# Kernel optimization log

Hardware: AMD Instinct MI355X
Metric: run time of the kernel (lower is better)

## Reference

```python
import jax, jax.numpy as jnp
import numpy as np

T, H, F, E, TOP_K = 4096, 2048, 4096, 8, 2  # tokens, d_model, d_ffn, experts, top_k


def setup_inputs() -> dict:
    key = jax.random.key(0)
    k_x, k_g, k_w1, k_w2 = jax.random.split(key, 4)
    hidden_states = jax.random.normal(k_x, (T, H), dtype=jnp.float32)
    # gate: nn.Linear(d_model, num_local_experts, bias=False) -> weight [E, H]
    gate_w = jax.random.normal(k_g, (E, H), dtype=jnp.float32) * 0.02
    # swiglu expert weights: per-expert up-proj [H, 2F] and down-proj [F, H]
    w1 = jax.random.normal(k_w1, (E, H, 2 * F), dtype=jnp.float32) * 0.02
    w2 = jax.random.normal(k_w2, (E, F, H), dtype=jnp.float32) * 0.02
    return {"hidden_states": hidden_states, "gate_w": gate_w, "w1": w1, "w2": w2}


def reference(hidden_states, gate_w, w1, w2):
    # 1) Gate routing: logits over local experts, top-k, softmax over the k scores
    gate_logits = hidden_states @ gate_w.T                      # [T, E]
    routing_scores, expert_ids = jax.lax.top_k(gate_logits, TOP_K)  # [T, K]
    routing_scores = jax.nn.softmax(routing_scores, axis=-1)    # [T, K]
    # 2-4) Dispatch -> grouped expert swiglu FFN -> weighted combine.
    #   num_ep_ranks=1 => local_eids == expert_ids; prototype dispatch does no quant.
    #   Loop over the small fixed expert set (E=8); each token's contribution is
    #   its summed routing weight for that expert (0 if not routed there).
    out = jnp.zeros_like(hidden_states)
    for e in range(E):
        tok_w = jnp.sum(routing_scores * (expert_ids == e), axis=-1)  # [T]
        h = hidden_states @ w1[e]                                     # [T, 2F]
        a, b = jnp.split(h, 2, axis=-1)
        y = (jax.nn.silu(a) * b) @ w2[e]                              # [T, H]
        out = out + tok_w[:, None] * y
    return out
```

## Files before the change

kernel.cpp:

```cpp
#include <hip/hip_runtime.h>

#define T_TOK 4096
#define H_DIM 2048
#define F_DIM 4096
#define E_NUM 8

typedef __attribute__((ext_vector_type(8))) short bf16x8;
typedef __attribute__((ext_vector_type(4))) float f32x4;
typedef __attribute__((ext_vector_type(4))) unsigned short us4;
typedef __attribute__((ext_vector_type(8))) unsigned short us8;

__device__ __forceinline__ unsigned short f2bf(float f) {
  union { float f; unsigned u; } v; v.f = f;
  unsigned r = v.u + 0x7FFFu + ((v.u >> 16) & 1u);
  return (unsigned short)(r >> 16);
}

__global__ void gate_kernel(const float* __restrict__ x, const float* __restrict__ gw,
                            int* __restrict__ counts, int* __restrict__ eids,
                            float* __restrict__ wts) {
  __shared__ int lc[E_NUM];
  const int tid = threadIdx.x;
  if (tid < E_NUM) lc[tid] = 0;
  __syncthreads();
  const int t = blockIdx.x * (blockDim.x >> 6) + (tid >> 6);
  const int lane = tid & 63;
  const float4* xr = (const float4*)(x + (size_t)t * H_DIM);
  float acc[E_NUM];
#pragma unroll
  for (int e = 0; e < E_NUM; ++e) acc[e] = 0.f;
#pragma unroll
  for (int j = 0; j < H_DIM / 256; ++j) {
    float4 xv = xr[lane + j * 64];
#pragma unroll
    for (int e = 0; e < E_NUM; ++e) {
      float4 gv = ((const float4*)(gw + (size_t)e * H_DIM))[lane + j * 64];
      acc[e] += xv.x * gv.x + xv.y * gv.y + xv.z * gv.z + xv.w * gv.w;
    }
  }
#pragma unroll
  for (int e = 0; e < E_NUM; ++e) {
    float v = acc[e];
    for (int off = 32; off > 0; off >>= 1) v += __shfl_xor(v, off, 64);
    acc[e] = v;
  }
  if (lane == 0) {
    float best = -1e30f, sec = -1e30f;
    int be = 0, se = 0;
#pragma unroll
    for (int e = 0; e < E_NUM; ++e) {
      float v = acc[e];
      if (v > best) { sec = best; se = be; best = v; be = e; }
      else if (v > sec) { sec = v; se = e; }
    }
    eids[2 * t] = be;
    eids[2 * t + 1] = se;
    float w0 = 1.f / (1.f + expf(sec - best));
    wts[2 * t] = w0;
    wts[2 * t + 1] = 1.f - w0;
    atomicAdd(&lc[be], 1);
    atomicAdd(&lc[se], 1);
  }
  __syncthreads();
  if (tid < E_NUM && lc[tid]) atomicAdd(&counts[tid], lc[tid]);
}

__global__ void scan_kernel(const int* __restrict__ counts, int* __restrict__ offsets,
                            int* __restrict__ cursors) {
  if (threadIdx.x == 0 && blockIdx.x == 0) {
    int s = 0;
    for (int e = 0; e < E_NUM; ++e) { offsets[e] = s; cursors[e] = s; s += counts[e]; }
  }
}

__global__ void assign_kernel(const int* __restrict__ eids, const float* __restrict__ wts,
                              int* __restrict__ cursors, int* __restrict__ tok_of_slot,
                              float* __restrict__ wslot) {
  __shared__ int lc[E_NUM], lb[E_NUM];
  const int tid = threadIdx.x;
  if (tid < E_NUM) lc[tid] = 0;
  __syncthreads();
  const int t = blockIdx.x * blockDim.x + tid;
  const int e0 = eids[2 * t], e1 = eids[2 * t + 1];
  const int p0 = atomicAdd(&lc[e0], 1);
  const int p1 = atomicAdd(&lc[e1], 1);
  __syncthreads();
  if (tid < E_NUM) lb[tid] = atomicAdd(&cursors[tid], lc[tid]);
  __syncthreads();
  const int s0 = lb[e0] + p0, s1 = lb[e1] + p1;
  tok_of_slot[s0] = t; wslot[s0] = wts[2 * t];
  tok_of_slot[s1] = t; wslot[s1] = wts[2 * t + 1];
}

__global__ __launch_bounds__(256, 2) void gemm_up(
    const float* __restrict__ x, const float* __restrict__ w1,
    const int* __restrict__ counts, const int* __restrict__ offsets,
    const int* __restrict__ tok_of_slot, unsigned short* __restrict__ act) {
  const int e = blockIdx.z;
  const int cnt = counts[e];
  const int m0 = blockIdx.y * 128;
  if (m0 >= cnt) return;
  const int base = offsets[e];
  const int nA = blockIdx.x * 128;

  __shared__ __align__(16) unsigned short As[128][40];
  __shared__ __align__(16) unsigned short Bs[2][128][40];

  const int tid = threadIdx.x;
  const int ak = (tid & 7) * 4;
  const float* aptr[4];
#pragma unroll
  for (int i = 0; i < 4; ++i) {
    int sm = m0 + (tid >> 3) + 32 * i;
    if (sm > cnt - 1) sm = cnt - 1;
    aptr[i] = x + (size_t)tok_of_slot[base + sm] * H_DIM + ak;
  }
  const int bn = tid & 127;
  const int bk = (tid >> 7) * 16;
  const float* wa = w1 + (size_t)e * H_DIM * (2 * F_DIM) + nA + bn;
  const float* wb = wa + F_DIM;

  const int lane = tid & 63;
  const int wv = tid >> 6;
  const int wr = (wv >> 1) * 64, wc = (wv & 1) * 64;
  const int fm = lane & 15, kq = lane >> 4;

  const f32x4 z = {0.f, 0.f, 0.f, 0.f};
  f32x4 acca[4][4], accb[4][4];
#pragma unroll
  for (int i = 0; i < 4; ++i)
#pragma unroll
    for (int j = 0; j < 4; ++j) { acca[i][j] = z; accb[i][j] = z; }

  for (int kt = 0; kt < H_DIM / 32; ++kt) {
    const int k0 = kt * 32;
#pragma unroll
    for (int i = 0; i < 4; ++i) {
      float4 v = *(const float4*)(aptr[i] + k0);
      us4 s; s.x = f2bf(v.x); s.y = f2bf(v.y); s.z = f2bf(v.z); s.w = f2bf(v.w);
      *(us4*)&As[(tid >> 3) + 32 * i][ak] = s;
    }
#pragma unroll
    for (int p = 0; p < 2; ++p) {
      const float* wp = p ? wb : wa;
#pragma unroll
      for (int q = 0; q < 4; ++q) {
        const int k = bk + q * 4;
        const size_t ro = (size_t)(k0 + k) * (2 * F_DIM);
        float v0 = wp[ro];
        float v1 = wp[ro + 2 * F_DIM];
        float v2 = wp[ro + 4 * F_DIM];
        float v3 = wp[ro + 6 * F_DIM];
        us4 s; s.x = f2bf(v0); s.y = f2bf(v1); s.z = f2bf(v2); s.w = f2bf(v3);
        *(us4*)&Bs[p][bn][k] = s;
      }
    }
    __syncthreads();
    bf16x8 af[4], bb[4];
#pragma unroll
    for (int i = 0; i < 4; ++i) af[i] = *(const bf16x8*)&As[wr + i * 16 + fm][kq * 8];
#pragma unroll
    for (int j = 0; j < 4; ++j) bb[j] = *(const bf16x8*)&Bs[0][wc + j * 16 + fm][kq * 8];
#pragma unroll
    for (int i = 0; i < 4; ++i)
#pragma unroll
      for (int j = 0; j < 4; ++j)
        acca[i][j] = __builtin_amdgcn_mfma_f32_16x16x32_bf16(af[i], bb[j], acca[i][j], 0, 0, 0);
#pragma unroll
    for (int j = 0; j < 4; ++j) bb[j] = *(const bf16x8*)&Bs[1][wc + j * 16 + fm][kq * 8];
#pragma unroll
    for (int i = 0; i < 4; ++i)
#pragma unroll
      for (int j = 0; j < 4; ++j)
        accb[i][j] = __builtin_amdgcn_mfma_f32_16x16x32_bf16(af[i], bb[j], accb[i][j], 0, 0, 0);
    __syncthreads();
  }

#pragma unroll
  for (int i = 0; i < 4; ++i) {
#pragma unroll
    for (int r = 0; r < 4; ++r) {
      const int lm = wr + i * 16 + kq * 4 + r;
      const int sm = m0 + lm;
      if (sm >= cnt) continue;
      const size_t ro = (size_t)(base + sm) * F_DIM + nA + wc + fm;
#pragma unroll
      for (int j = 0; j < 4; ++j) {
        float a = acca[i][j][r];
        float b = accb[i][j][r];
        float s = a / (1.f + __expf(-a)) * b;
        act[ro + (size_t)j * 16] = f2bf(s);
      }
    }
  }
}

__global__ __launch_bounds__(256, 2) void gemm_down(
    const unsigned short* __restrict__ act, const float* __restrict__ w2,
    const int* __restrict__ counts, const int* __restrict__ offsets,
    const int* __restrict__ tok_of_slot, const float* __restrict__ wslot,
    float* __restrict__ out) {
  const int e = blockIdx.z;
  const int cnt = counts[e];
  const int m0 = blockIdx.y * 128;
  if (m0 >= cnt) return;
  const int base = offsets[e];
  const int nB = blockIdx.x * 128;

  __shared__ __align__(16) unsigned short As[128][40];
  __shared__ __align__(16) unsigned short Bs[128][40];

  const int tid = threadIdx.x;
  const int ak8 = (tid & 3) * 8;
  const unsigned short* aptr[2];
#pragma unroll
  for (int i = 0; i < 2; ++i) {
    int sm = m0 + (tid >> 2) + 64 * i;
    if (sm > cnt - 1) sm = cnt - 1;
    aptr[i] = act + (size_t)(base + sm) * F_DIM + ak8;
  }
  const int bn = tid & 127;
  const int bk = (tid >> 7) * 16;
  const float* wp = w2 + (size_t)e * F_DIM * H_DIM + nB + bn;

  const int lane = tid & 63;
  const int wv = tid >> 6;
  const int wr = (wv >> 1) * 64, wc = (wv & 1) * 64;
  const int fm = lane & 15, kq = lane >> 4;

  const f32x4 z = {0.f, 0.f, 0.f, 0.f};
  f32x4 acc[4][4];
#pragma unroll
  for (int i = 0; i < 4; ++i)
#pragma unroll
    for (int j = 0; j < 4; ++j) acc[i][j] = z;

  for (int kt = 0; kt < F_DIM / 32; ++kt) {
    const int k0 = kt * 32;
#pragma unroll
    for (int i = 0; i < 2; ++i)
      *(us8*)&As[(tid >> 2) + 64 * i][ak8] = *(const us8*)(aptr[i] + k0);
#pragma unroll
    for (int q = 0; q < 4; ++q) {
      const int k = bk + q * 4;
      const size_t ro = (size_t)(k0 + k) * H_DIM;
      float v0 = wp[ro];
      float v1 = wp[ro + H_DIM];
      float v2 = wp[ro + 2 * H_DIM];
      float v3 = wp[ro + 3 * H_DIM];
      us4 s; s.x = f2bf(v0); s.y = f2bf(v1); s.z = f2bf(v2); s.w = f2bf(v3);
      *(us4*)&Bs[bn][k] = s;
    }
    __syncthreads();
    bf16x8 af[4], bb[4];
#pragma unroll
    for (int i = 0; i < 4; ++i) af[i] = *(const bf16x8*)&As[wr + i * 16 + fm][kq * 8];
#pragma unroll
    for (int j = 0; j < 4; ++j) bb[j] = *(const bf16x8*)&Bs[wc + j * 16 + fm][kq * 8];
#pragma unroll
    for (int i = 0; i < 4; ++i)
#pragma unroll
      for (int j = 0; j < 4; ++j)
        acc[i][j] = __builtin_amdgcn_mfma_f32_16x16x32_bf16(af[i], bb[j], acc[i][j], 0, 0, 0);
    __syncthreads();
  }

#pragma unroll
  for (int i = 0; i < 4; ++i) {
#pragma unroll
    for (int r = 0; r < 4; ++r) {
      const int lm = wr + i * 16 + kq * 4 + r;
      const int sm = m0 + lm;
      if (sm >= cnt) continue;
      const int slot = base + sm;
      const int tok = tok_of_slot[slot];
      const float wg = wslot[slot];
      float* orow = out + (size_t)tok * H_DIM + nB + wc + fm;
#pragma unroll
      for (int j = 0; j < 4; ++j)
        atomicAdd(&orow[j * 16], wg * acc[i][j][r]);
    }
  }
}

extern "C" void kernel_launch(void* const* d_in, const int* in_sizes, int n_in,
                              void* d_out, int out_size, void* d_ws, size_t ws_size,
                              hipStream_t stream) {
  const float* x  = (const float*)d_in[0];
  const float* gw = (const float*)d_in[1];
  const float* w1 = (const float*)d_in[2];
  const float* w2 = (const float*)d_in[3];
  float* out = (float*)d_out;
  char* ws = (char*)d_ws;

  int*   counts      = (int*)(ws + 0);
  int*   offsets     = (int*)(ws + 64);
  int*   cursors     = (int*)(ws + 128);
  int*   eids        = (int*)(ws + 1024);
  float* wts         = (float*)(ws + 65536);
  int*   tok_of_slot = (int*)(ws + 131072);
  float* wslot       = (float*)(ws + 196608);
  unsigned short* act = (unsigned short*)(ws + 262144);

  hipMemsetAsync(ws, 0, 256, stream);
  hipMemsetAsync(d_out, 0, (size_t)T_TOK * H_DIM * sizeof(float), stream);

  gate_kernel<<<T_TOK / 8, 512, 0, stream>>>(x, gw, counts, eids, wts);
  scan_kernel<<<1, 64, 0, stream>>>(counts, offsets, cursors);
  assign_kernel<<<T_TOK / 256, 256, 0, stream>>>(eids, wts, cursors, tok_of_slot, wslot);
  gemm_up<<<dim3(F_DIM / 128, T_TOK / 128, E_NUM), 256, 0, stream>>>(
      x, w1, counts, offsets, tok_of_slot, act);
  gemm_down<<<dim3(H_DIM / 128, T_TOK / 128, E_NUM), 256, 0, stream>>>(
      act, w2, counts, offsets, tok_of_slot, wslot, out);
}
```

Before: 1.608 ms.

## Pre-convert weights to transposed bf16 and stream tiles via global_load_lds

Adds pre-passes that convert x to bf16 and transpose-convert w1/w2 into K-contiguous bf16 layouts each call. The GEMMs then load tiles straight into LDS with global_load_lds into a swizzled layout, removing per-tile fp32 loads, conversions and strided weight reads. The down-projection now writes per-slot bf16 outputs, and a separate combine kernel does the weighted sum instead of atomics, which also drops the output memset. This costs extra passes over roughly 400MB of weights per call and a large workspace, and falls back to the old path when the workspace is too small.

```diff
diff --git a/kernel.cpp b/kernel.cpp
--- a/kernel.cpp
+++ b/kernel.cpp
@@ -15,6 +15,15 @@
   unsigned r = v.u + 0x7FFFu + ((v.u >> 16) & 1u);
   return (unsigned short)(r >> 16);
 }
+__device__ __forceinline__ float bf2f(unsigned short s) {
+  union { unsigned u; float f; } v; v.u = ((unsigned)s) << 16;
+  return v.f;
+}
+
+#define GL2LDS16(g, l)                                                        \
+  __builtin_amdgcn_global_load_lds(                                           \
+      (__attribute__((address_space(1))) void*)(g),                           \
+      (__attribute__((address_space(3))) void*)(l), 16, 0, 0)
 
 __global__ void gate_kernel(const float* __restrict__ x, const float* __restrict__ gw,
                             int* __restrict__ counts, int* __restrict__ eids,
@@ -75,7 +84,7 @@
 
 __global__ void assign_kernel(const int* __restrict__ eids, const float* __restrict__ wts,
                               int* __restrict__ cursors, int* __restrict__ tok_of_slot,
-                              float* __restrict__ wslot) {
+                              float* __restrict__ wslot, int* __restrict__ slot_of_tok) {
   __shared__ int lc[E_NUM], lb[E_NUM];
   const int tid = threadIdx.x;
   if (tid < E_NUM) lc[tid] = 0;
@@ -90,9 +99,268 @@
   const int s0 = lb[e0] + p0, s1 = lb[e1] + p1;
   tok_of_slot[s0] = t; wslot[s0] = wts[2 * t];
   tok_of_slot[s1] = t; wslot[s1] = wts[2 * t + 1];
-}
-
-__global__ __launch_bounds__(256, 2) void gemm_up(
+  slot_of_tok[2 * t] = s0; slot_of_tok[2 * t + 1] = s1;
+}
+
+__global__ void convert_x_kernel(const float* __restrict__ in, unsigned short* __restrict__ out) {
+  const size_t i8 = ((size_t)blockIdx.x * blockDim.x + threadIdx.x) * 8;
+  float4 a = *(const float4*)(in + i8);
+  float4 b = *(const float4*)(in + i8 + 4);
+  us8 o;
+  o[0] = f2bf(a.x); o[1] = f2bf(a.y); o[2] = f2bf(a.z); o[3] = f2bf(a.w);
+  o[4] = f2bf(b.x); o[5] = f2bf(b.y); o[6] = f2bf(b.z); o[7] = f2bf(b.w);
+  *(us8*)(out + i8) = o;
+}
+
+__global__ void transpose_cvt(const float* __restrict__ in, unsigned short* __restrict__ out,
+                              int K, int N) {
+  __shared__ __align__(16) unsigned short tile[64 * 64];
+  const int e = blockIdx.z;
+  const int n0 = blockIdx.x * 64;
+  const int k0 = blockIdx.y * 64;
+  const float* ib = in + (size_t)e * K * N;
+  unsigned short* ob = out + (size_t)e * N * K;
+  const int tid = threadIdx.x;
+  const int c = (tid & 15) * 4;
+#pragma unroll
+  for (int pp = 0; pp < 2; ++pp) {
+    const int P = (tid >> 4) + 16 * pp;
+    const int kk = 2 * P;
+    float4 f0 = *(const float4*)(ib + (size_t)(k0 + kk) * N + n0 + c);
+    float4 f1 = *(const float4*)(ib + (size_t)(k0 + kk + 1) * N + n0 + c);
+    const float v0[4] = {f0.x, f0.y, f0.z, f0.w};
+    const float v1[4] = {f1.x, f1.y, f1.z, f1.w};
+    const int q = P >> 2, j = P & 3;
+#pragma unroll
+    for (int i = 0; i < 4; ++i) {
+      const int m = c + i;
+      const int slot = (q + m + (m >> 2)) & 7;
+      unsigned pk = (unsigned)f2bf(v0[i]) | ((unsigned)f2bf(v1[i]) << 16);
+      *(unsigned*)&tile[m * 64 + slot * 8 + j * 2] = pk;
+    }
+  }
+  __syncthreads();
+  const int n = tid >> 2;
+#pragma unroll
+  for (int qq = 0; qq < 2; ++qq) {
+    const int q = 2 * (tid & 3) + qq;
+    const int slot = (q + n + (n >> 2)) & 7;
+    us8 v = *(const us8*)&tile[n * 64 + slot * 8];
+    *(us8*)(ob + (size_t)(n0 + n) * K + k0 + q * 8) = v;
+  }
+}
+
+
+__global__ __launch_bounds__(256, 2) void gemm_up_f(
+    const unsigned short* __restrict__ xb, const unsigned short* __restrict__ w1t,
+    const int* __restrict__ counts, const int* __restrict__ offsets,
+    const int* __restrict__ tok_of_slot, unsigned short* __restrict__ act) {
+  const int e = blockIdx.z;
+  const int cnt = counts[e];
+  const int m0 = blockIdx.y * 128;
+  if (m0 >= cnt) return;
+  const int base = offsets[e];
+  const int nA = blockIdx.x * 128;
+
+  __shared__ __align__(16) unsigned short As[128 * 32];
+  __shared__ __align__(16) unsigned short Bs[2][128 * 32];
+
+  const int tid = threadIdx.x;
+  const int wv = tid >> 6;
+  const int lane = tid & 63;
+
+  const unsigned short* aga[2];
+  unsigned short* alds[2];
+#pragma unroll
+  for (int i = 0; i < 2; ++i) {
+    const int r = wv * 32 + i * 16 + (lane >> 2);
+    const int g = ((lane & 3) - (r >> 1)) & 3;
+    int sm = m0 + r; if (sm > cnt - 1) sm = cnt - 1;
+    aga[i] = xb + (size_t)tok_of_slot[base + sm] * H_DIM + g * 8;
+    alds[i] = &As[(wv * 32 + i * 16) * 32];
+  }
+  const unsigned short* bga[4];
+  unsigned short* blds[4];
+  {
+    const int p = wv >> 1;
+#pragma unroll
+    for (int i = 0; i < 4; ++i) {
+      const int r = (wv & 1) * 64 + i * 16 + (lane >> 2);
+      const int g = ((lane & 3) - (r >> 1)) & 3;
+      const int ncol = nA + r + p * F_DIM;
+      bga[i] = w1t + (size_t)e * (2 * F_DIM) * H_DIM + (size_t)ncol * H_DIM + g * 8;
+      blds[i] = &Bs[p][((wv & 1) * 64 + i * 16) * 32];
+    }
+  }
+
+  const int wr = (wv >> 1) * 64, wc = (wv & 1) * 64;
+  const int fm = lane & 15, kq = lane >> 4;
+  int aoff[4], boff[4];
+#pragma unroll
+  for (int i = 0; i < 4; ++i) {
+    const int ra = wr + i * 16 + fm;
+    aoff[i] = ra * 32 + ((kq + (ra >> 1)) & 3) * 8;
+    const int rb = wc + i * 16 + fm;
+    boff[i] = rb * 32 + ((kq + (rb >> 1)) & 3) * 8;
+  }
+
+  const f32x4 z = {0.f, 0.f, 0.f, 0.f};
+  f32x4 acca[4][4], accb[4][4];
+#pragma unroll
+  for (int i = 0; i < 4; ++i)
+#pragma unroll
+    for (int j = 0; j < 4; ++j) { acca[i][j] = z; accb[i][j] = z; }
+
+  for (int kt = 0; kt < H_DIM / 32; ++kt) {
+    const int k0 = kt * 32;
+#pragma unroll
+    for (int i = 0; i < 2; ++i) GL2LDS16(aga[i] + k0, alds[i]);
+#pragma unroll
+    for (int i = 0; i < 4; ++i) GL2LDS16(bga[i] + k0, blds[i]);
+    __syncthreads();
+    bf16x8 af[4], bb[4];
+#pragma unroll
+    for (int i = 0; i < 4; ++i) af[i] = *(const bf16x8*)&As[aoff[i]];
+#pragma unroll
+    for (int j = 0; j < 4; ++j) bb[j] = *(const bf16x8*)&Bs[0][boff[j]];
+#pragma unroll
+    for (int i = 0; i < 4; ++i)
+#pragma unroll
+      for (int j = 0; j < 4; ++j)
+        acca[i][j] = __builtin_amdgcn_mfma_f32_16x16x32_bf16(af[i], bb[j], acca[i][j], 0, 0, 0);
+#pragma unroll
+    for (int j = 0; j < 4; ++j) bb[j] = *(const bf16x8*)&Bs[1][boff[j]];
+#pragma unroll
+    for (int i = 0; i < 4; ++i)
+#pragma unroll
+      for (int j = 0; j < 4; ++j)
+        accb[i][j] = __builtin_amdgcn_mfma_f32_16x16x32_bf16(af[i], bb[j], accb[i][j], 0, 0, 0);
+    __syncthreads();
+  }
+
+#pragma unroll
+  for (int i = 0; i < 4; ++i) {
+#pragma unroll
+    for (int r = 0; r < 4; ++r) {
+      const int lm = wr + i * 16 + kq * 4 + r;
+      const int sm = m0 + lm;
+      if (sm >= cnt) continue;
+      const size_t ro = (size_t)(base + sm) * F_DIM + nA + wc + fm;
+#pragma unroll
+      for (int j = 0; j < 4; ++j) {
+        float a = acca[i][j][r];
+        float b = accb[i][j][r];
+        float s = a / (1.f + __expf(-a)) * b;
+        act[ro + (size_t)j * 16] = f2bf(s);
+      }
+    }
+  }
+}
+
+__global__ __launch_bounds__(256, 2) void gemm_down_f(
+    const unsigned short* __restrict__ act, const unsigned short* __restrict__ w2t,
+    const int* __restrict__ counts, const int* __restrict__ offsets,
+    unsigned short* __restrict__ yslot) {
+  const int e = blockIdx.z;
+  const int cnt = counts[e];
+  const int m0 = blockIdx.y * 128;
+  if (m0 >= cnt) return;
+  const int base = offsets[e];
+  const int nB = blockIdx.x * 128;
+
+  __shared__ __align__(16) unsigned short As[128 * 32];
+  __shared__ __align__(16) unsigned short Bs[128 * 32];
+
+  const int tid = threadIdx.x;
+  const int wv = tid >> 6;
+  const int lane = tid & 63;
+
+  const unsigned short* aga[2];
+  unsigned short* alds[2];
+  const unsigned short* bga[2];
+  unsigned short* blds[2];
+#pragma unroll
+  for (int i = 0; i < 2; ++i) {
+    const int r = wv * 32 + i * 16 + (lane >> 2);
+    const int g = ((lane & 3) - (r >> 1)) & 3;
+    int sm = m0 + r; if (sm > cnt - 1) sm = cnt - 1;
+    aga[i] = act + (size_t)(base + sm) * F_DIM + g * 8;
+    alds[i] = &As[(wv * 32 + i * 16) * 32];
+    bga[i] = w2t + (size_t)e * H_DIM * F_DIM + (size_t)(nB + r) * F_DIM + g * 8;
+    blds[i] = &Bs[(wv * 32 + i * 16) * 32];
+  }
+
+  const int wr = (wv >> 1) * 64, wc = (wv & 1) * 64;
+  const int fm = lane & 15, kq = lane >> 4;
+  int aoff[4], boff[4];
+#pragma unroll
+  for (int i = 0; i < 4; ++i) {
+    const int ra = wr + i * 16 + fm;
+    aoff[i] = ra * 32 + ((kq + (ra >> 1)) & 3) * 8;
+    const int rb = wc + i * 16 + fm;
+    boff[i] = rb * 32 + ((kq + (rb >> 1)) & 3) * 8;
+  }
+
+  const f32x4 z = {0.f, 0.f, 0.f, 0.f};
+  f32x4 acc[4][4];
+#pragma unroll
+  for (int i = 0; i < 4; ++i)
+#pragma unroll
+    for (int j = 0; j < 4; ++j) acc[i][j] = z;
+
+  for (int kt = 0; kt < F_DIM / 32; ++kt) {
+    const int k0 = kt * 32;
+#pragma unroll
+    for (int i = 0; i < 2; ++i) GL2LDS16(aga[i] + k0, alds[i]);
+#pragma unroll
+    for (int i = 0; i < 2; ++i) GL2LDS16(bga[i] + k0, blds[i]);
+    __syncthreads();
+    bf16x8 af[4], bb[4];
+#pragma unroll
+    for (int i = 0; i < 4; ++i) af[i] = *(const bf16x8*)&As[aoff[i]];
+#pragma unroll
+    for (int j = 0; j < 4; ++j) bb[j] = *(const bf16x8*)&Bs[boff[j]];
+#pragma unroll
+    for (int i = 0; i < 4; ++i)
+#pragma unroll
+      for (int j = 0; j < 4; ++j)
+        acc[i][j] = __builtin_amdgcn_mfma_f32_16x16x32_bf16(af[i], bb[j], acc[i][j], 0, 0, 0);
+    __syncthreads();
+  }
+
+#pragma unroll
+  for (int i = 0; i < 4; ++i) {
+#pragma unroll
+    for (int r = 0; r < 4; ++r) {
+      const int lm = wr + i * 16 + kq * 4 + r;
+      const int sm = m0 + lm;
+      if (sm >= cnt) continue;
+      const size_t ro = (size_t)(base + sm) * H_DIM + nB + wc + fm;
+#pragma unroll
+      for (int j = 0; j < 4; ++j)
+        yslot[ro + (size_t)j * 16] = f2bf(acc[i][j][r]);
+    }
+  }
+}
+
+__global__ void combine_kernel(const unsigned short* __restrict__ yslot,
+                               const int* __restrict__ slot_of_tok,
+                               const float* __restrict__ wslot, float* __restrict__ out) {
+  const int t = blockIdx.x;
+  const int c = threadIdx.x * 8;
+  const int s0 = slot_of_tok[2 * t], s1 = slot_of_tok[2 * t + 1];
+  const float w0 = wslot[s0], w1 = wslot[s1];
+  us8 y0 = *(const us8*)(yslot + (size_t)s0 * H_DIM + c);
+  us8 y1 = *(const us8*)(yslot + (size_t)s1 * H_DIM + c);
+  float o[8];
+#pragma unroll
+  for (int i = 0; i < 8; ++i) o[i] = w0 * bf2f(y0[i]) + w1 * bf2f(y1[i]);
+  float* op = out + (size_t)t * H_DIM + c;
+  *(float4*)op = make_float4(o[0], o[1], o[2], o[3]);
+  *(float4*)(op + 4) = make_float4(o[4], o[5], o[6], o[7]);
+}
+
+__global__ __launch_bounds__(256, 2) void gemm_up_s(
     const float* __restrict__ x, const float* __restrict__ w1,
     const int* __restrict__ counts, const int* __restrict__ offsets,
     const int* __restrict__ tok_of_slot, unsigned short* __restrict__ act) {
@@ -102,10 +370,8 @@
   if (m0 >= cnt) return;
   const int base = offsets[e];
   const int nA = blockIdx.x * 128;
-
   __shared__ __align__(16) unsigned short As[128][40];
   __shared__ __align__(16) unsigned short Bs[2][128][40];
-
   const int tid = threadIdx.x;
   const int ak = (tid & 7) * 4;
   const float* aptr[4];
@@ -119,19 +385,16 @@
   const int bk = (tid >> 7) * 16;
   const float* wa = w1 + (size_t)e * H_DIM * (2 * F_DIM) + nA + bn;
   const float* wb = wa + F_DIM;
-
   const int lane = tid & 63;
   const int wv = tid >> 6;
   const int wr = (wv >> 1) * 64, wc = (wv & 1) * 64;
   const int fm = lane & 15, kq = lane >> 4;
-
   const f32x4 z = {0.f, 0.f, 0.f, 0.f};
   f32x4 acca[4][4], accb[4][4];
 #pragma unroll
   for (int i = 0; i < 4; ++i)
 #pragma unroll
     for (int j = 0; j < 4; ++j) { acca[i][j] = z; accb[i][j] = z; }
-
   for (int kt = 0; kt < H_DIM / 32; ++kt) {
     const int k0 = kt * 32;
 #pragma unroll
@@ -175,7 +438,6 @@
         accb[i][j] = __builtin_amdgcn_mfma_f32_16x16x32_bf16(af[i], bb[j], accb[i][j], 0, 0, 0);
     __syncthreads();
   }
-
 #pragma unroll
   for (int i = 0; i < 4; ++i) {
 #pragma unroll
@@ -195,7 +457,7 @@
   }
 }
 
-__global__ __launch_bounds__(256, 2) void gemm_down(
+__global__ __launch_bounds__(256, 2) void gemm_down_s(
     const unsigned short* __restrict__ act, const float* __restrict__ w2,
     const int* __restrict__ counts, const int* __restrict__ offsets,
     const int* __restrict__ tok_of_slot, const float* __restrict__ wslot,
@@ -206,10 +468,8 @@
   if (m0 >= cnt) return;
   const int base = offsets[e];
   const int nB = blockIdx.x * 128;
-
   __shared__ __align__(16) unsigned short As[128][40];
   __shared__ __align__(16) unsigned short Bs[128][40];
-
   const int tid = threadIdx.x;
   const int ak8 = (tid & 3) * 8;
   const unsigned short* aptr[2];
@@ -222,19 +482,16 @@
   const int bn = tid & 127;
   const int bk = (tid >> 7) * 16;
   const float* wp = w2 + (size_t)e * F_DIM * H_DIM + nB + bn;
-
   const int lane = tid & 63;
   const int wv = tid >> 6;
   const int wr = (wv >> 1) * 64, wc = (wv & 1) * 64;
   const int fm = lane & 15, kq = lane >> 4;
-
   const f32x4 z = {0.f, 0.f, 0.f, 0.f};
   f32x4 acc[4][4];
 #pragma unroll
   for (int i = 0; i < 4; ++i)
 #pragma unroll
     for (int j = 0; j < 4; ++j) acc[i][j] = z;
-
   for (int kt = 0; kt < F_DIM / 32; ++kt) {
     const int k0 = kt * 32;
 #pragma unroll
@@ -264,7 +521,6 @@
         acc[i][j] = __builtin_amdgcn_mfma_f32_16x16x32_bf16(af[i], bb[j], acc[i][j], 0, 0, 0);
     __syncthreads();
   }
-
 #pragma unroll
   for (int i = 0; i < 4; ++i) {
 #pragma unroll
@@ -300,16 +556,37 @@
   float* wts         = (float*)(ws + 65536);
   int*   tok_of_slot = (int*)(ws + 131072);
   float* wslot       = (float*)(ws + 196608);
+  int*   slot_of_tok = (int*)(ws + 229376);
   unsigned short* act = (unsigned short*)(ws + 262144);
-
-  hipMemsetAsync(ws, 0, 256, stream);
-  hipMemsetAsync(d_out, 0, (size_t)T_TOK * H_DIM * sizeof(float), stream);
+  unsigned short* xb    = (unsigned short*)(ws + 67371008);
+  unsigned short* yslot = (unsigned short*)(ws + 84148224);
+  unsigned short* w1t   = (unsigned short*)(ws + 117702656);
+  unsigned short* w2t   = (unsigned short*)(ws + 386138112);
+  const size_t NEED_FAST = 520355840;
+
+  hipMemsetAsync(ws, 0, 1024, stream);
 
   gate_kernel<<<T_TOK / 8, 512, 0, stream>>>(x, gw, counts, eids, wts);
   scan_kernel<<<1, 64, 0, stream>>>(counts, offsets, cursors);
-  assign_kernel<<<T_TOK / 256, 256, 0, stream>>>(eids, wts, cursors, tok_of_slot, wslot);
-  gemm_up<<<dim3(F_DIM / 128, T_TOK / 128, E_NUM), 256, 0, stream>>>(
-      x, w1, counts, offsets, tok_of_slot, act);
-  gemm_down<<<dim3(H_DIM / 128, T_TOK / 128, E_NUM), 256, 0, stream>>>(
-      act, w2, counts, offsets, tok_of_slot, wslot, out);
-}
+  assign_kernel<<<T_TOK / 256, 256, 0, stream>>>(eids, wts, cursors, tok_of_slot, wslot,
+                                                 slot_of_tok);
+
+  if (ws_size >= NEED_FAST) {
+    convert_x_kernel<<<(T_TOK * H_DIM / 8) / 256, 256, 0, stream>>>(x, xb);
+    transpose_cvt<<<dim3(2 * F_DIM / 64, H_DIM / 64, E_NUM), 256, 0, stream>>>(
+        w1, w1t, H_DIM, 2 * F_DIM);
+    transpose_cvt<<<dim3(H_DIM / 64, F_DIM / 64, E_NUM), 256, 0, stream>>>(
+        w2, w2t, F_DIM, H_DIM);
+    gemm_up_f<<<dim3(F_DIM / 128, T_TOK / 128, E_NUM), 256, 0, stream>>>(
+        xb, w1t, counts, offsets, tok_of_slot, act);
+    gemm_down_f<<<dim3(H_DIM / 128, T_TOK / 128, E_NUM), 256, 0, stream>>>(
+        act, w2t, counts, offsets, yslot);
+    combine_kernel<<<T_TOK, 256, 0, stream>>>(yslot, slot_of_tok, wslot, out);
+  } else {
+    hipMemsetAsync(d_out, 0, (size_t)T_TOK * H_DIM * sizeof(float), stream);
+    gemm_up_s<<<dim3(F_DIM / 128, T_TOK / 128, E_NUM), 256, 0, stream>>>(
+        x, w1, counts, offsets, tok_of_slot, act);
+    gemm_down_s<<<dim3(H_DIM / 128, T_TOK / 128, E_NUM), 256, 0, stream>>>(
+        act, w2, counts, offsets, tok_of_slot, wslot, out);
+  }
+}
```

Result: faster. 1.537 ms (-4.4%).
